# Performance work log

Measured on AMD Instinct MI355X. Metric: run time of the kernel, lower is better.

The kernel has to match this reference:

```python
import jax, jax.numpy as jnp
import numpy as np

INPUT_DIM = 512
HIDDEN_DIM = 1024
OUTPUT_DIM = 512
BATCH = 256
SEQ = 512


def setup_inputs() -> dict:
    key = jax.random.key(0)
    ks = jax.random.split(key, 7)
    s_ih = 1.0 / np.sqrt(HIDDEN_DIM)
    x = jax.random.normal(ks[0], (BATCH, SEQ, INPUT_DIM), dtype=jnp.float32)
    # PyTorch nn.LSTM params: weight_ih [4H, I], weight_hh [4H, H], biases [4H]
    W_ih = jax.random.uniform(ks[1], (4 * HIDDEN_DIM, INPUT_DIM), minval=-s_ih, maxval=s_ih, dtype=jnp.float32)
    W_hh = jax.random.uniform(ks[2], (4 * HIDDEN_DIM, HIDDEN_DIM), minval=-s_ih, maxval=s_ih, dtype=jnp.float32)
    b_ih = jax.random.uniform(ks[3], (4 * HIDDEN_DIM,), minval=-s_ih, maxval=s_ih, dtype=jnp.float32)
    b_hh = jax.random.uniform(ks[4], (4 * HIDDEN_DIM,), minval=-s_ih, maxval=s_ih, dtype=jnp.float32)
    s_fc = 1.0 / np.sqrt(HIDDEN_DIM)
    W_fc = jax.random.uniform(ks[5], (OUTPUT_DIM, HIDDEN_DIM), minval=-s_fc, maxval=s_fc, dtype=jnp.float32)
    b_fc = jax.random.uniform(ks[6], (OUTPUT_DIM,), minval=-s_fc, maxval=s_fc, dtype=jnp.float32)
    return {"x": x, "W_ih": W_ih, "W_hh": W_hh, "b_ih": b_ih, "b_hh": b_hh, "W_fc": W_fc, "b_fc": b_fc}


def _lstm_last_hidden(x, W_ih, W_hh, b_ih, b_hh):
    B = x.shape[0]
    H = W_hh.shape[1]
    # Precompute input projections for all timesteps: [T, B, 4H]
    xW = jnp.einsum('bti,gi->tbg', x, W_ih) + (b_ih + b_hh)

    def step(carry, xw_t):
        h, c = carry
        z = xw_t + h @ W_hh.T  # [B, 4H]
        i, f, g, o = jnp.split(z, 4, axis=-1)  # PyTorch gate order i,f,g,o
        i = jax.nn.sigmoid(i)
        f = jax.nn.sigmoid(f)
        g = jnp.tanh(g)
        o = jax.nn.sigmoid(o)
        c = f * c + i * g
        h = o * jnp.tanh(c)
        return (h, c), None

    h0 = jnp.zeros((B, H), dtype=x.dtype)
    c0 = jnp.zeros((B, H), dtype=x.dtype)
    (hT, _), _ = jax.lax.scan(step, (h0, c0), xW)
    return hT  # last timestep hidden == out[:, -1, :]


def reference(x, W_ih, W_hh, b_ih, b_hh, W_fc, b_fc):
    hT = _lstm_last_hidden(x, W_ih, W_hh, b_ih, b_hh)
    return hT @ W_fc.T + b_fc  # [B, output_dim]
```

## Files before the change

### kernel.cpp

```cpp
#include <hip/hip_runtime.h>
#include <stdint.h>


#define T_STEPS 512

typedef __bf16 bf16x8 __attribute__((ext_vector_type(8)));
typedef float  f32x4  __attribute__((ext_vector_type(4)));

__device__ __forceinline__ uint16_t f2bf(float f) {
  uint32_t u = __float_as_uint(f);
  u += 0x7fffu + ((u >> 16) & 1u);
  return (uint16_t)(u >> 16);
}
__device__ __forceinline__ float sigmoid_f(float z) {
  return 1.0f / (1.0f + __expf(-z));
}
__device__ __forceinline__ float tanh_f(float x) {
  float ax = __builtin_fabsf(x);
  float e  = __expf(-2.0f * ax);
  float r  = (1.0f - e) / (1.0f + e);
  return __builtin_copysignf(r, x);
}


__global__ __launch_bounds__(256) void prep_w(const float* __restrict__ Wih,
                                              const float* __restrict__ Whh,
                                              uint16_t* __restrict__ wp,
                                              int* __restrict__ flags) {
  if (blockIdx.x < 16) {
    __hip_atomic_store(&flags[blockIdx.x * 256 + threadIdx.x], 0,
                       __ATOMIC_RELAXED, __HIP_MEMORY_SCOPE_AGENT);
  }
  int idx = blockIdx.x * 256 + threadIdx.x;
  int l = idx & 63;
  int r = idx >> 6;
  int s = r % 48; r /= 48;
  int q = r & 1;  r >>= 1;
  int w = r & 3;  r >>= 2;
  int jt = r;
  int row = w * 1024 + jt * 32 + q * 16 + (l & 15);
  int kb  = s * 32 + (l >> 4) * 8;
  const float* src = (kb < 1024) ? (Whh + (size_t)row * 1024 + kb)
                                 : (Wih + (size_t)row * 512 + (kb - 1024));
  uint32_t d0 = (uint32_t)f2bf(src[0]) | ((uint32_t)f2bf(src[1]) << 16);
  uint32_t d1 = (uint32_t)f2bf(src[2]) | ((uint32_t)f2bf(src[3]) << 16);
  uint32_t d2 = (uint32_t)f2bf(src[4]) | ((uint32_t)f2bf(src[5]) << 16);
  uint32_t d3 = (uint32_t)f2bf(src[6]) | ((uint32_t)f2bf(src[7]) << 16);
  *(uint4*)(wp + (size_t)idx * 8) = make_uint4(d0, d1, d2, d3);
}

__global__ __launch_bounds__(256) void prep_x(const float* __restrict__ x,
                                              uint16_t* __restrict__ xp) {
  int idx = blockIdx.x * 256 + threadIdx.x;
  int l = idx & 63;
  int r = idx >> 6;
  int mt = r & 1;  r >>= 1;
  int ks = r & 15; r >>= 4;
  int bt = r & 7;  r >>= 3;
  int t  = r;
  int b = bt * 32 + mt * 16 + (l & 15);
  int k = ks * 32 + (l >> 4) * 8;
  const float* src = x + ((size_t)b * 512 + t) * 512 + k;
  uint32_t d0 = (uint32_t)f2bf(src[0]) | ((uint32_t)f2bf(src[1]) << 16);
  uint32_t d1 = (uint32_t)f2bf(src[2]) | ((uint32_t)f2bf(src[3]) << 16);
  uint32_t d2 = (uint32_t)f2bf(src[4]) | ((uint32_t)f2bf(src[5]) << 16);
  uint32_t d3 = (uint32_t)f2bf(src[6]) | ((uint32_t)f2bf(src[7]) << 16);
  *(uint4*)(xp + (size_t)idx * 8) = make_uint4(d0, d1, d2, d3);
}

__global__ __launch_bounds__(256, 1) void lstm_main(
    const uint16_t* __restrict__ wpack,
    const uint16_t* __restrict__ xpack,
    uint16_t* __restrict__ hpack,
    float* __restrict__ hfinal,
    int* flags,
    const float* __restrict__ bih,
    const float* __restrict__ bhh,
    const float* __restrict__ Wfc,
    const float* __restrict__ bfc,
    float* __restrict__ out) {
  extern __shared__ char smem[];

  const int tid = threadIdx.x;
  const int w   = tid >> 6;
  const int l   = tid & 63;
  const int jt  = blockIdx.x >> 3;
  const int bt  = blockIdx.x & 7;

  char* const hbuf  = smem;
  char* const xbuf0 = smem + 65536;
  char* const xbuf1 = smem + 98304;
  float* const zl   = (float*)(smem + 131072);

  int* const flag_self = flags + ((bt * 32 + jt) << 4);
  const int* const flag_poll = flags + ((bt * 32 + (l & 31)) << 4);
  int spin_budget = 2000000;

  bf16x8 fb[2][48];
#pragma unroll
  for (int q = 0; q < 2; ++q) {
#pragma unroll
    for (int s = 0; s < 48; ++s) {
      union { uint4 u; bf16x8 b; } cv;
      cv.u = *(const uint4*)(wpack +
              (size_t)(((jt * 4 + w) * 2 + q) * 48 + s) * 512 + (size_t)l * 8);
      fb[q][s] = cv.b;
    }
  }

  float bias0, bias1;
  {
    int u0b = jt * 32 + (l & 15);
    bias0 = bih[w * 1024 + u0b]      + bhh[w * 1024 + u0b];
    bias1 = bih[w * 1024 + u0b + 16] + bhh[w * 1024 + u0b + 16];
  }

  const int umt = tid >> 7;
  const int ul  = (tid >> 1) & 63;
  const int uj  = (tid & 1) * 4;
  const int um  = umt * 16 + (ul & 15);
  const int uu0 = (ul >> 4) * 8 + uj;
  float c0 = 0.f, c1 = 0.f, c2 = 0.f, c3 = 0.f;

  {
    const uint16_t* src = xpack + (size_t)bt * 16384;
#pragma unroll
    for (int i = 0; i < 8; ++i) {
      int ci = w * 8 + i;
      __builtin_amdgcn_global_load_lds(
          (const __attribute__((address_space(1))) void*)(src + (size_t)ci * 512 + (size_t)l * 8),
          (__attribute__((address_space(3))) void*)(xbuf0 + ci * 1024), 16, 0, 0);
    }
  }
  __syncthreads();

  for (int t = 0; t < T_STEPS; ++t) {
    if (t + 1 < T_STEPS) {
      const uint16_t* src = xpack + (size_t)((t + 1) * 8 + bt) * 16384;
      char* dst = ((t + 1) & 1) ? xbuf1 : xbuf0;
#pragma unroll
      for (int i = 0; i < 8; ++i) {
        int ci = w * 8 + i;
        __builtin_amdgcn_global_load_lds(
            (const __attribute__((address_space(1))) void*)(src + (size_t)ci * 512 + (size_t)l * 8),
            (__attribute__((address_space(3))) void*)(dst + ci * 1024), 16, 0, 0);
      }
    }

    f32x4 acc[2][2];
#pragma unroll
    for (int mt = 0; mt < 2; ++mt)
#pragma unroll
      for (int q = 0; q < 2; ++q) acc[mt][q] = (f32x4){0.f, 0.f, 0.f, 0.f};

    const char* xc = (t & 1) ? xbuf1 : xbuf0;

#pragma unroll
    for (int s = 0; s < 8; ++s) {
#pragma unroll
      for (int mt = 0; mt < 2; ++mt) {
        bf16x8 a = *(const bf16x8*)(xc + ((s * 2 + mt) * 64 + l) * 16);
        acc[mt][0] = __builtin_amdgcn_mfma_f32_16x16x32_bf16(a, fb[0][32 + s], acc[mt][0], 0, 0, 0);
        acc[mt][1] = __builtin_amdgcn_mfma_f32_16x16x32_bf16(a, fb[1][32 + s], acc[mt][1], 0, 0, 0);
      }
    }

    if (t > 0) {
      if (tid < 64) {
        for (;;) {
          int v = __hip_atomic_load(flag_poll, __ATOMIC_RELAXED,
                                    __HIP_MEMORY_SCOPE_AGENT);
          if (__all(v >= t)) break;
          if (--spin_budget < 0) break;
          __builtin_amdgcn_s_sleep(1);
        }
      }
      __syncthreads();
      const uint16_t* hs = hpack + (size_t)(((t - 1) & 1) * 8 + bt) * 32768;
#pragma unroll
      for (int i = 0; i < 16; ++i) {
        int ci = w * 16 + i;
        __builtin_amdgcn_global_load_lds(
            (const __attribute__((address_space(1))) void*)(hs + (size_t)ci * 512 + (size_t)l * 8),
            (__attribute__((address_space(3))) void*)(hbuf + ci * 1024), 16, 0, 17);
      }
    }

#pragma unroll
    for (int s = 8; s < 16; ++s) {
#pragma unroll
      for (int mt = 0; mt < 2; ++mt) {
        bf16x8 a = *(const bf16x8*)(xc + ((s * 2 + mt) * 64 + l) * 16);
        acc[mt][0] = __builtin_amdgcn_mfma_f32_16x16x32_bf16(a, fb[0][32 + s], acc[mt][0], 0, 0, 0);
        acc[mt][1] = __builtin_amdgcn_mfma_f32_16x16x32_bf16(a, fb[1][32 + s], acc[mt][1], 0, 0, 0);
      }
    }

    __syncthreads();
    if (t > 0) {
#pragma unroll
      for (int s = 0; s < 32; ++s) {
#pragma unroll
        for (int mt = 0; mt < 2; ++mt) {
          bf16x8 a = *(const bf16x8*)(hbuf + ((s * 2 + mt) * 64 + l) * 16);
          acc[mt][0] = __builtin_amdgcn_mfma_f32_16x16x32_bf16(a, fb[0][s], acc[mt][0], 0, 0, 0);
          acc[mt][1] = __builtin_amdgcn_mfma_f32_16x16x32_bf16(a, fb[1][s], acc[mt][1], 0, 0, 0);
        }
      }
    }

#pragma unroll
    for (int mt = 0; mt < 2; ++mt) {
#pragma unroll
      for (int q = 0; q < 2; ++q) {
        f32x4 v = acc[mt][q];
        float bq = q ? bias1 : bias0;
#pragma unroll
        for (int r = 0; r < 4; ++r) {
          float z = v[r] + bq;
          float a = (w == 2) ? tanh_f(z) : sigmoid_f(z);
          int m  = mt * 16 + (l >> 4) * 4 + r;
          int uu = q * 16 + (l & 15);
          zl[(w * 32 + m) * 36 + uu] = a;
        }
      }
    }
    __syncthreads();

    {
      const f32x4 gi = *(const f32x4*)&zl[(0 * 32 + um) * 36 + uu0];
      const f32x4 gf = *(const f32x4*)&zl[(1 * 32 + um) * 36 + uu0];
      const f32x4 gg = *(const f32x4*)&zl[(2 * 32 + um) * 36 + uu0];
      const f32x4 go = *(const f32x4*)&zl[(3 * 32 + um) * 36 + uu0];
      c0 = gf[0] * c0 + gi[0] * gg[0];
      c1 = gf[1] * c1 + gi[1] * gg[1];
      c2 = gf[2] * c2 + gi[2] * gg[2];
      c3 = gf[3] * c3 + gi[3] * gg[3];
      float h0 = go[0] * tanh_f(c0);
      float h1 = go[1] * tanh_f(c1);
      float h2 = go[2] * tanh_f(c2);
      float h3 = go[3] * tanh_f(c3);
      uint32_t p0 = (uint32_t)f2bf(h0) | ((uint32_t)f2bf(h1) << 16);
      uint32_t p1 = (uint32_t)f2bf(h2) | ((uint32_t)f2bf(h3) << 16);
      unsigned long long pv = ((unsigned long long)p1 << 32) | (unsigned long long)p0;
      uint16_t* hp = hpack +
          (size_t)((((t & 1) * 8 + bt) * 32 + jt) * 2 + umt) * 512 + (size_t)ul * 8 + uj;
      __hip_atomic_store((unsigned long long*)hp, pv,
                         __ATOMIC_RELAXED, __HIP_MEMORY_SCOPE_AGENT);
      if (t == T_STEPS - 1) {
        unsigned long long q0 = ((unsigned long long)__float_as_uint(h1) << 32) |
                                (unsigned long long)__float_as_uint(h0);
        unsigned long long q1 = ((unsigned long long)__float_as_uint(h3) << 32) |
                                (unsigned long long)__float_as_uint(h2);
        unsigned long long* fp = (unsigned long long*)
            &hfinal[(size_t)(bt * 32 + um) * 1024 + jt * 32 + uu0];
        __hip_atomic_store(fp,     q0, __ATOMIC_RELAXED, __HIP_MEMORY_SCOPE_AGENT);
        __hip_atomic_store(fp + 1, q1, __ATOMIC_RELAXED, __HIP_MEMORY_SCOPE_AGENT);
      }
    }

    asm volatile("s_waitcnt vmcnt(0)" ::: "memory");
    __syncthreads();
    if (tid == 0) {
      __hip_atomic_store(flag_self, t + 1, __ATOMIC_RELAXED,
                         __HIP_MEMORY_SCOPE_AGENT);
    }
  }

  if (tid < 64) {
    for (;;) {
      int v = __hip_atomic_load(flag_poll, __ATOMIC_RELAXED,
                                __HIP_MEMORY_SCOPE_AGENT);
      if (__all(v >= T_STEPS)) break;
      if (--spin_budget < 0) break;
      __builtin_amdgcn_s_sleep(1);
    }
  }
  __syncthreads();

  float* const hl = (float*)smem;
  {
    const unsigned long long* hq =
        (const unsigned long long*)(hfinal + (size_t)bt * 32 * 1024);
#pragma unroll 4
    for (int i = 0; i < 64; ++i) {
      int d   = i * 256 + tid;
      int row = d >> 9;
      int c2  = d & 511;
      unsigned long long v = __hip_atomic_load(hq + (size_t)row * 512 + c2,
                                               __ATOMIC_RELAXED, __HIP_MEMORY_SCOPE_AGENT);
      *(unsigned long long*)&hl[row * 1028 + c2 * 2] = v;
    }
  }
  __syncthreads();
  {
    const int bl = tid >> 3;
    const int oo = tid & 7;
    const int o0 = jt * 16 + oo * 2;
    float a0 = 0.f, a1 = 0.f;
    const float* hrow = &hl[bl * 1028];
    const float* w0p  = Wfc + (size_t)o0 * 1024;
    const float* w1p  = w0p + 1024;
#pragma unroll 8
    for (int k = 0; k < 1024; k += 4) {
      f32x4 hv = *(const f32x4*)&hrow[k];
      f32x4 w0 = *(const f32x4*)&w0p[k];
      f32x4 w1 = *(const f32x4*)&w1p[k];
      a0 += hv[0] * w0[0] + hv[1] * w0[1] + hv[2] * w0[2] + hv[3] * w0[3];
      a1 += hv[0] * w1[0] + hv[1] * w1[1] + hv[2] * w1[2] + hv[3] * w1[3];
    }
    int b = bt * 32 + bl;
    out[(size_t)b * 512 + o0]     = a0 + bfc[o0];
    out[(size_t)b * 512 + o0 + 1] = a1 + bfc[o0 + 1];
  }
}

extern "C" void kernel_launch(void* const* d_in, const int* in_sizes, int n_in,
                              void* d_out, int out_size, void* d_ws, size_t ws_size,
                              hipStream_t stream) {
  const float* x   = (const float*)d_in[0];
  const float* Wih = (const float*)d_in[1];
  const float* Whh = (const float*)d_in[2];
  const float* bih = (const float*)d_in[3];
  const float* bhh = (const float*)d_in[4];
  const float* Wfc = (const float*)d_in[5];
  const float* bfc = (const float*)d_in[6];
  float* out = (float*)d_out;

  char* ws = (char*)d_ws;
  uint16_t* wp  = (uint16_t*)(ws);
  uint16_t* xp  = (uint16_t*)(ws + 12582912);
  uint16_t* hp  = (uint16_t*)(ws + 146800640);
  float*    hf  = (float*)   (ws + 147849216);
  int*      fl  = (int*)     (ws + 148897792);

  (void)hipFuncSetAttribute((const void*)lstm_main,
                            hipFuncAttributeMaxDynamicSharedMemorySize, 149504);

  hipLaunchKernelGGL(prep_w, dim3(3072), dim3(256), 0, stream, Wih, Whh, wp, fl);
  hipLaunchKernelGGL(prep_x, dim3(32768), dim3(256), 0, stream, x, xp);
  hipLaunchKernelGGL(lstm_main, dim3(256), dim3(256), 149504, stream,
                     wp, xp, hp, hf, fl, bih, bhh, Wfc, bfc, out);
}
```

Before: 3.688 ms.

## Pipeline recurrent h loads into four groups with partial vmcnt waits

The per-step h-state load into LDS is reordered so that each wave's chunks interleave across four groups. The h-projection MFMA loop is split into four stages, each waiting only on its own group's loads with a partial vmcnt and a barrier, so compute on early chunks overlaps the remaining loads. The next-timestep x prefetch is moved after the flag wait so it no longer competes with the h loads on the critical path. This relies on the ordering of vmcnt counters, and mixing inline-asm waitcnt with the compiler's own scheduling is fragile.

New measurement: 4.005 ms. 1.09x slower.

```diff
diff --git a/kernel.cpp b/kernel.cpp
--- a/kernel.cpp
+++ b/kernel.cpp
@@ -68,6 +68,25 @@
   *(uint4*)(xp + (size_t)idx * 8) = make_uint4(d0, d1, d2, d3);
 }
 
+#define H_GROUP(g, VM)                                                        \
+  do {                                                                        \
+    asm volatile("s_waitcnt vmcnt(" #VM ")" ::: "memory");                    \
+    __builtin_amdgcn_s_barrier();                                             \
+    asm volatile("" ::: "memory");                                            \
+    _Pragma("unroll")                                                         \
+    for (int so = 0; so < 8; ++so) {                                          \
+      const int s = (g) * 8 + so;                                             \
+      _Pragma("unroll")                                                       \
+      for (int mt = 0; mt < 2; ++mt) {                                        \
+        bf16x8 a = *(const bf16x8*)(hbuf + ((s * 2 + mt) * 64 + l) * 16);     \
+        acc[mt][0] = __builtin_amdgcn_mfma_f32_16x16x32_bf16(                 \
+            a, fb[0][s], acc[mt][0], 0, 0, 0);                                \
+        acc[mt][1] = __builtin_amdgcn_mfma_f32_16x16x32_bf16(                 \
+            a, fb[1][s], acc[mt][1], 0, 0, 0);                                \
+      }                                                                       \
+    }                                                                         \
+  } while (0)
+
 __global__ __launch_bounds__(256, 1) void lstm_main(
     const uint16_t* __restrict__ wpack,
     const uint16_t* __restrict__ xpack,
@@ -135,18 +154,6 @@
   __syncthreads();
 
   for (int t = 0; t < T_STEPS; ++t) {
-    if (t + 1 < T_STEPS) {
-      const uint16_t* src = xpack + (size_t)((t + 1) * 8 + bt) * 16384;
-      char* dst = ((t + 1) & 1) ? xbuf1 : xbuf0;
-#pragma unroll
-      for (int i = 0; i < 8; ++i) {
-        int ci = w * 8 + i;
-        __builtin_amdgcn_global_load_lds(
-            (const __attribute__((address_space(1))) void*)(src + (size_t)ci * 512 + (size_t)l * 8),
-            (__attribute__((address_space(3))) void*)(dst + ci * 1024), 16, 0, 0);
-      }
-    }
-
     f32x4 acc[2][2];
 #pragma unroll
     for (int mt = 0; mt < 2; ++mt)
@@ -176,10 +183,25 @@
         }
       }
       __syncthreads();
+    }
+
+    if (t + 1 < T_STEPS) {
+      const uint16_t* src = xpack + (size_t)((t + 1) * 8 + bt) * 16384;
+      char* dst = ((t + 1) & 1) ? xbuf1 : xbuf0;
+#pragma unroll
+      for (int i = 0; i < 8; ++i) {
+        int ci = w * 8 + i;
+        __builtin_amdgcn_global_load_lds(
+            (const __attribute__((address_space(1))) void*)(src + (size_t)ci * 512 + (size_t)l * 8),
+            (__attribute__((address_space(3))) void*)(dst + ci * 1024), 16, 0, 0);
+      }
+    }
+
+    if (t > 0) {
       const uint16_t* hs = hpack + (size_t)(((t - 1) & 1) * 8 + bt) * 32768;
 #pragma unroll
       for (int i = 0; i < 16; ++i) {
-        int ci = w * 16 + i;
+        int ci = 16 * (i >> 2) + w * 4 + (i & 3);
         __builtin_amdgcn_global_load_lds(
             (const __attribute__((address_space(1))) void*)(hs + (size_t)ci * 512 + (size_t)l * 8),
             (__attribute__((address_space(3))) void*)(hbuf + ci * 1024), 16, 0, 17);
@@ -196,17 +218,13 @@
       }
     }
 
-    __syncthreads();
     if (t > 0) {
-#pragma unroll
-      for (int s = 0; s < 32; ++s) {
-#pragma unroll
-        for (int mt = 0; mt < 2; ++mt) {
-          bf16x8 a = *(const bf16x8*)(hbuf + ((s * 2 + mt) * 64 + l) * 16);
-          acc[mt][0] = __builtin_amdgcn_mfma_f32_16x16x32_bf16(a, fb[0][s], acc[mt][0], 0, 0, 0);
-          acc[mt][1] = __builtin_amdgcn_mfma_f32_16x16x32_bf16(a, fb[1][s], acc[mt][1], 0, 0, 0);
-        }
-      }
+      H_GROUP(0, 12);
+      H_GROUP(1, 8);
+      H_GROUP(2, 4);
+      H_GROUP(3, 0);
+    } else {
+      __syncthreads();
     }
 
 #pragma unroll
```

## Split LSTM step K-reduction across two wave groups with 512-thread blocks

Applied to the files above, without the earlier changes.

Doubles the block to 512 threads (8 waves). Each gate's K-dimension is split between two wave halves, so each wave holds half the weight fragments in registers. Partial sums are reduced through LDS before the activation, and the cell update and FC epilogue are spread over more threads. The next-step x prefetch moves to after the flag wait, and the spin budget is lowered. The aim is to shorten the serial per-step latency by halving the MFMA chain per wave, at the cost of an extra LDS exchange and barrier each step.

Result: slower. 5.453 ms (+47.8%).

```diff
diff --git a/kernel.cpp b/kernel.cpp
--- a/kernel.cpp
+++ b/kernel.cpp
@@ -6,6 +6,7 @@
 
 typedef __bf16 bf16x8 __attribute__((ext_vector_type(8)));
 typedef float  f32x4  __attribute__((ext_vector_type(4)));
+typedef float  f32x2  __attribute__((ext_vector_type(2)));
 
 __device__ __forceinline__ uint16_t f2bf(float f) {
   uint32_t u = __float_as_uint(f);
@@ -68,7 +69,7 @@
   *(uint4*)(xp + (size_t)idx * 8) = make_uint4(d0, d1, d2, d3);
 }
 
-__global__ __launch_bounds__(256, 1) void lstm_main(
+__global__ __launch_bounds__(512, 2) void lstm_main(
     const uint16_t* __restrict__ wpack,
     const uint16_t* __restrict__ xpack,
     uint16_t* __restrict__ hpack,
@@ -82,7 +83,9 @@
   extern __shared__ char smem[];
 
   const int tid = threadIdx.x;
-  const int w   = tid >> 6;
+  const int w8  = tid >> 6;
+  const int g8  = w8 & 3;
+  const int p8  = w8 >> 2;
   const int l   = tid & 63;
   const int jt  = blockIdx.x >> 3;
   const int bt  = blockIdx.x & 7;
@@ -94,39 +97,40 @@
 
   int* const flag_self = flags + ((bt * 32 + jt) << 4);
   const int* const flag_poll = flags + ((bt * 32 + (l & 31)) << 4);
-  int spin_budget = 2000000;
-
-  bf16x8 fb[2][48];
+  int spin_budget = 150000;
+
+  bf16x8 fb[2][24];
 #pragma unroll
   for (int q = 0; q < 2; ++q) {
 #pragma unroll
-    for (int s = 0; s < 48; ++s) {
+    for (int j = 0; j < 24; ++j) {
+      int s = (j < 16) ? (p8 * 16 + j) : (32 + p8 * 8 + (j - 16));
       union { uint4 u; bf16x8 b; } cv;
       cv.u = *(const uint4*)(wpack +
-              (size_t)(((jt * 4 + w) * 2 + q) * 48 + s) * 512 + (size_t)l * 8);
-      fb[q][s] = cv.b;
+              (size_t)(((jt * 4 + g8) * 2 + q) * 48 + s) * 512 + (size_t)l * 8);
+      fb[q][j] = cv.b;
     }
   }
 
   float bias0, bias1;
   {
     int u0b = jt * 32 + (l & 15);
-    bias0 = bih[w * 1024 + u0b]      + bhh[w * 1024 + u0b];
-    bias1 = bih[w * 1024 + u0b + 16] + bhh[w * 1024 + u0b + 16];
-  }
-
-  const int umt = tid >> 7;
-  const int ul  = (tid >> 1) & 63;
-  const int uj  = (tid & 1) * 4;
+    bias0 = bih[g8 * 1024 + u0b]      + bhh[g8 * 1024 + u0b];
+    bias1 = bih[g8 * 1024 + u0b + 16] + bhh[g8 * 1024 + u0b + 16];
+  }
+
+  const int umt = tid >> 8;
+  const int ul  = (tid >> 2) & 63;
+  const int uj  = (tid & 3) * 2;
   const int um  = umt * 16 + (ul & 15);
   const int uu0 = (ul >> 4) * 8 + uj;
-  float c0 = 0.f, c1 = 0.f, c2 = 0.f, c3 = 0.f;
+  float c0 = 0.f, c1 = 0.f;
 
   {
     const uint16_t* src = xpack + (size_t)bt * 16384;
 #pragma unroll
-    for (int i = 0; i < 8; ++i) {
-      int ci = w * 8 + i;
+    for (int i = 0; i < 4; ++i) {
+      int ci = w8 * 4 + i;
       __builtin_amdgcn_global_load_lds(
           (const __attribute__((address_space(1))) void*)(src + (size_t)ci * 512 + (size_t)l * 8),
           (__attribute__((address_space(3))) void*)(xbuf0 + ci * 1024), 16, 0, 0);
@@ -135,18 +139,6 @@
   __syncthreads();
 
   for (int t = 0; t < T_STEPS; ++t) {
-    if (t + 1 < T_STEPS) {
-      const uint16_t* src = xpack + (size_t)((t + 1) * 8 + bt) * 16384;
-      char* dst = ((t + 1) & 1) ? xbuf1 : xbuf0;
-#pragma unroll
-      for (int i = 0; i < 8; ++i) {
-        int ci = w * 8 + i;
-        __builtin_amdgcn_global_load_lds(
-            (const __attribute__((address_space(1))) void*)(src + (size_t)ci * 512 + (size_t)l * 8),
-            (__attribute__((address_space(3))) void*)(dst + ci * 1024), 16, 0, 0);
-      }
-    }
-
     f32x4 acc[2][2];
 #pragma unroll
     for (int mt = 0; mt < 2; ++mt)
@@ -156,12 +148,13 @@
     const char* xc = (t & 1) ? xbuf1 : xbuf0;
 
 #pragma unroll
-    for (int s = 0; s < 8; ++s) {
+    for (int jj = 0; jj < 4; ++jj) {
+      int ks = p8 * 8 + jj;
 #pragma unroll
       for (int mt = 0; mt < 2; ++mt) {
-        bf16x8 a = *(const bf16x8*)(xc + ((s * 2 + mt) * 64 + l) * 16);
-        acc[mt][0] = __builtin_amdgcn_mfma_f32_16x16x32_bf16(a, fb[0][32 + s], acc[mt][0], 0, 0, 0);
-        acc[mt][1] = __builtin_amdgcn_mfma_f32_16x16x32_bf16(a, fb[1][32 + s], acc[mt][1], 0, 0, 0);
+        bf16x8 a = *(const bf16x8*)(xc + ((ks * 2 + mt) * 64 + l) * 16);
+        acc[mt][0] = __builtin_amdgcn_mfma_f32_16x16x32_bf16(a, fb[0][16 + jj], acc[mt][0], 0, 0, 0);
+        acc[mt][1] = __builtin_amdgcn_mfma_f32_16x16x32_bf16(a, fb[1][16 + jj], acc[mt][1], 0, 0, 0);
       }
     }
 
@@ -176,10 +169,25 @@
         }
       }
       __syncthreads();
+    }
+
+    if (t + 1 < T_STEPS) {
+      const uint16_t* src = xpack + (size_t)((t + 1) * 8 + bt) * 16384;
+      char* dst = ((t + 1) & 1) ? xbuf1 : xbuf0;
+#pragma unroll
+      for (int i = 0; i < 4; ++i) {
+        int ci = w8 * 4 + i;
+        __builtin_amdgcn_global_load_lds(
+            (const __attribute__((address_space(1))) void*)(src + (size_t)ci * 512 + (size_t)l * 8),
+            (__attribute__((address_space(3))) void*)(dst + ci * 1024), 16, 0, 0);
+      }
+    }
+
+    if (t > 0) {
       const uint16_t* hs = hpack + (size_t)(((t - 1) & 1) * 8 + bt) * 32768;
 #pragma unroll
-      for (int i = 0; i < 16; ++i) {
-        int ci = w * 16 + i;
+      for (int i = 0; i < 8; ++i) {
+        int ci = w8 * 8 + i;
         __builtin_amdgcn_global_load_lds(
             (const __attribute__((address_space(1))) void*)(hs + (size_t)ci * 512 + (size_t)l * 8),
             (__attribute__((address_space(3))) void*)(hbuf + ci * 1024), 16, 0, 17);
@@ -187,75 +195,83 @@
     }
 
 #pragma unroll
-    for (int s = 8; s < 16; ++s) {
+    for (int jj = 4; jj < 8; ++jj) {
+      int ks = p8 * 8 + jj;
 #pragma unroll
       for (int mt = 0; mt < 2; ++mt) {
-        bf16x8 a = *(const bf16x8*)(xc + ((s * 2 + mt) * 64 + l) * 16);
-        acc[mt][0] = __builtin_amdgcn_mfma_f32_16x16x32_bf16(a, fb[0][32 + s], acc[mt][0], 0, 0, 0);
-        acc[mt][1] = __builtin_amdgcn_mfma_f32_16x16x32_bf16(a, fb[1][32 + s], acc[mt][1], 0, 0, 0);
+        bf16x8 a = *(const bf16x8*)(xc + ((ks * 2 + mt) * 64 + l) * 16);
+        acc[mt][0] = __builtin_amdgcn_mfma_f32_16x16x32_bf16(a, fb[0][16 + jj], acc[mt][0], 0, 0, 0);
+        acc[mt][1] = __builtin_amdgcn_mfma_f32_16x16x32_bf16(a, fb[1][16 + jj], acc[mt][1], 0, 0, 0);
       }
     }
 
     __syncthreads();
     if (t > 0) {
 #pragma unroll
-      for (int s = 0; s < 32; ++s) {
+      for (int j = 0; j < 16; ++j) {
+        int s = p8 * 16 + j;
 #pragma unroll
         for (int mt = 0; mt < 2; ++mt) {
           bf16x8 a = *(const bf16x8*)(hbuf + ((s * 2 + mt) * 64 + l) * 16);
-          acc[mt][0] = __builtin_amdgcn_mfma_f32_16x16x32_bf16(a, fb[0][s], acc[mt][0], 0, 0, 0);
-          acc[mt][1] = __builtin_amdgcn_mfma_f32_16x16x32_bf16(a, fb[1][s], acc[mt][1], 0, 0, 0);
+          acc[mt][0] = __builtin_amdgcn_mfma_f32_16x16x32_bf16(a, fb[0][j], acc[mt][0], 0, 0, 0);
+          acc[mt][1] = __builtin_amdgcn_mfma_f32_16x16x32_bf16(a, fb[1][j], acc[mt][1], 0, 0, 0);
         }
       }
     }
 
-#pragma unroll
-    for (int mt = 0; mt < 2; ++mt) {
+    {
+      const int mto = 1 - p8;
 #pragma unroll
       for (int q = 0; q < 2; ++q) {
-        f32x4 v = acc[mt][q];
+        f32x4 v = acc[mto][q];
+#pragma unroll
+        for (int r = 0; r < 4; ++r) {
+          int m  = mto * 16 + (l >> 4) * 4 + r;
+          int uu = q * 16 + (l & 15);
+          zl[(g8 * 32 + m) * 36 + uu] = v[r];
+        }
+      }
+    }
+    __syncthreads();
+
+    {
+      const int mtk = p8;
+#pragma unroll
+      for (int q = 0; q < 2; ++q) {
+        f32x4 v = acc[mtk][q];
         float bq = q ? bias1 : bias0;
 #pragma unroll
         for (int r = 0; r < 4; ++r) {
-          float z = v[r] + bq;
-          float a = (w == 2) ? tanh_f(z) : sigmoid_f(z);
-          int m  = mt * 16 + (l >> 4) * 4 + r;
+          int m  = mtk * 16 + (l >> 4) * 4 + r;
           int uu = q * 16 + (l & 15);
-          zl[(w * 32 + m) * 36 + uu] = a;
+          float z = v[r] + zl[(g8 * 32 + m) * 36 + uu] + bq;
+          float a = (g8 == 2) ? tanh_f(z) : sigmoid_f(z);
+          zl[(g8 * 32 + m) * 36 + uu] = a;
         }
       }
     }
     __syncthreads();
 
     {
-      const f32x4 gi = *(const f32x4*)&zl[(0 * 32 + um) * 36 + uu0];
-      const f32x4 gf = *(const f32x4*)&zl[(1 * 32 + um) * 36 + uu0];
-      const f32x4 gg = *(const f32x4*)&zl[(2 * 32 + um) * 36 + uu0];
-      const f32x4 go = *(const f32x4*)&zl[(3 * 32 + um) * 36 + uu0];
+      const f32x2 gi = *(const f32x2*)&zl[(0 * 32 + um) * 36 + uu0];
+      const f32x2 gf = *(const f32x2*)&zl[(1 * 32 + um) * 36 + uu0];
+      const f32x2 gg = *(const f32x2*)&zl[(2 * 32 + um) * 36 + uu0];
+      const f32x2 go = *(const f32x2*)&zl[(3 * 32 + um) * 36 + uu0];
       c0 = gf[0] * c0 + gi[0] * gg[0];
       c1 = gf[1] * c1 + gi[1] * gg[1];
-      c2 = gf[2] * c2 + gi[2] * gg[2];
-      c3 = gf[3] * c3 + gi[3] * gg[3];
       float h0 = go[0] * tanh_f(c0);
       float h1 = go[1] * tanh_f(c1);
-      float h2 = go[2] * tanh_f(c2);
-      float h3 = go[3] * tanh_f(c3);
-      uint32_t p0 = (uint32_t)f2bf(h0) | ((uint32_t)f2bf(h1) << 16);
-      uint32_t p1 = (uint32_t)f2bf(h2) | ((uint32_t)f2bf(h3) << 16);
-      unsigned long long pv = ((unsigned long long)p1 << 32) | (unsigned long long)p0;
+      uint32_t pv = (uint32_t)f2bf(h0) | ((uint32_t)f2bf(h1) << 16);
       uint16_t* hp = hpack +
           (size_t)((((t & 1) * 8 + bt) * 32 + jt) * 2 + umt) * 512 + (size_t)ul * 8 + uj;
-      __hip_atomic_store((unsigned long long*)hp, pv,
+      __hip_atomic_store((uint32_t*)hp, pv,
                          __ATOMIC_RELAXED, __HIP_MEMORY_SCOPE_AGENT);
       if (t == T_STEPS - 1) {
         unsigned long long q0 = ((unsigned long long)__float_as_uint(h1) << 32) |
                                 (unsigned long long)__float_as_uint(h0);
-        unsigned long long q1 = ((unsigned long long)__float_as_uint(h3) << 32) |
-                                (unsigned long long)__float_as_uint(h2);
         unsigned long long* fp = (unsigned long long*)
             &hfinal[(size_t)(bt * 32 + um) * 1024 + jt * 32 + uu0];
-        __hip_atomic_store(fp,     q0, __ATOMIC_RELAXED, __HIP_MEMORY_SCOPE_AGENT);
-        __hip_atomic_store(fp + 1, q1, __ATOMIC_RELAXED, __HIP_MEMORY_SCOPE_AGENT);
+        __hip_atomic_store(fp, q0, __ATOMIC_RELAXED, __HIP_MEMORY_SCOPE_AGENT);
       }
     }
 
@@ -283,8 +299,8 @@
     const unsigned long long* hq =
         (const unsigned long long*)(hfinal + (size_t)bt * 32 * 1024);
 #pragma unroll 4
-    for (int i = 0; i < 64; ++i) {
-      int d   = i * 256 + tid;
+    for (int i = 0; i < 32; ++i) {
+      int d   = i * 512 + tid;
       int row = d >> 9;
       int c2  = d & 511;
       unsigned long long v = __hip_atomic_load(hq + (size_t)row * 512 + c2,
@@ -294,24 +310,20 @@
   }
   __syncthreads();
   {
-    const int bl = tid >> 3;
-    const int oo = tid & 7;
-    const int o0 = jt * 16 + oo * 2;
-    float a0 = 0.f, a1 = 0.f;
+    const int bl = tid >> 4;
+    const int oo = tid & 15;
+    const int o0 = jt * 16 + oo;
+    float a0 = 0.f;
     const float* hrow = &hl[bl * 1028];
     const float* w0p  = Wfc + (size_t)o0 * 1024;
-    const float* w1p  = w0p + 1024;
 #pragma unroll 8
     for (int k = 0; k < 1024; k += 4) {
       f32x4 hv = *(const f32x4*)&hrow[k];
       f32x4 w0 = *(const f32x4*)&w0p[k];
-      f32x4 w1 = *(const f32x4*)&w1p[k];
       a0 += hv[0] * w0[0] + hv[1] * w0[1] + hv[2] * w0[2] + hv[3] * w0[3];
-      a1 += hv[0] * w1[0] + hv[1] * w1[1] + hv[2] * w1[2] + hv[3] * w1[3];
     }
     int b = bt * 32 + bl;
-    out[(size_t)b * 512 + o0]     = a0 + bfc[o0];
-    out[(size_t)b * 512 + o0 + 1] = a1 + bfc[o0 + 1];
+    out[(size_t)b * 512 + o0] = a0 + bfc[o0];
   }
 }
 
@@ -339,6 +351,6 @@
 
   hipLaunchKernelGGL(prep_w, dim3(3072), dim3(256), 0, stream, Wih, Whh, wp, fl);
   hipLaunchKernelGGL(prep_x, dim3(32768), dim3(256), 0, stream, x, xp);
-  hipLaunchKernelGGL(lstm_main, dim3(256), dim3(256), 149504, stream,
+  hipLaunchKernelGGL(lstm_main, dim3(256), dim3(512), 149504, stream,
                      wp, xp, hp, hf, fl, bih, bhh, Wfc, bfc, out);
 }
```

## Split LSTM batch tile into two halves to overlap hidden-state exchange

Applied to the files above, without the earlier changes.

Each timestep now runs as two half-steps, one per 16-row half of the block's batch tile. Each half has its own ready flags and its own LDS h buffer. While one half computes its recurrent MFMAs and gate update, the h of the other half is fetched from global memory once its producers signal readiness, so the grid-wide exchange latency is meant to hide behind compute. The cost is twice as many barriers and flag publications per step, and smaller vector stores. The spin-wait timeout is also cut sharply, which risks a silent early break if producers fall behind.

After: 4.030 ms. 1.09x slower.

```diff
diff --git a/kernel.cpp b/kernel.cpp
--- a/kernel.cpp
+++ b/kernel.cpp
@@ -6,6 +6,7 @@
 
 typedef __bf16 bf16x8 __attribute__((ext_vector_type(8)));
 typedef float  f32x4  __attribute__((ext_vector_type(4)));
+typedef float  f32x2  __attribute__((ext_vector_type(2)));
 
 __device__ __forceinline__ uint16_t f2bf(float f) {
   uint32_t u = __float_as_uint(f);
@@ -68,6 +69,120 @@
   *(uint4*)(xp + (size_t)idx * 8) = make_uint4(d0, d1, d2, d3);
 }
 
+#define HALF_STEP(X, DO_LOAD, S_LOAD, DO_PREF, C0, C1)                        \
+  do {                                                                        \
+    f32x4 acc0 = (f32x4){0.f, 0.f, 0.f, 0.f};                                 \
+    f32x4 acc1 = (f32x4){0.f, 0.f, 0.f, 0.f};                                 \
+    const char* xc = (t & 1) ? xbuf1 : xbuf0;                                 \
+                                           \
+    _Pragma("unroll")                                                         \
+    for (int s = 0; s < 16; ++s) {                                            \
+      bf16x8 a = *(const bf16x8*)(xc + ((s * 2 + (X)) * 64 + l) * 16);        \
+      acc0 = __builtin_amdgcn_mfma_f32_16x16x32_bf16(a, fb[0][32 + s], acc0, 0, 0, 0); \
+      acc1 = __builtin_amdgcn_mfma_f32_16x16x32_bf16(a, fb[1][32 + s], acc1, 0, 0, 0); \
+    }                                                                         \
+                            \
+    if (t > 0) {                                                              \
+      const char* hb = (X) ? hbufB : hbufA;                                   \
+      _Pragma("unroll")                                                       \
+      for (int s = 0; s < 32; ++s) {                                          \
+        bf16x8 a = *(const bf16x8*)(hb + (s * 64 + l) * 16);                  \
+        acc0 = __builtin_amdgcn_mfma_f32_16x16x32_bf16(a, fb[0][s], acc0, 0, 0, 0); \
+        acc1 = __builtin_amdgcn_mfma_f32_16x16x32_bf16(a, fb[1][s], acc1, 0, 0, 0); \
+      }                                                                       \
+    }                                                                         \
+           \
+    if (DO_LOAD) {                                                            \
+      const int tgt = (S_LOAD) + 1;                                           \
+      const int* fp = (X) ? flag_pollA : flag_pollB;                          \
+      for (;;) {                                                              \
+        int v = __hip_atomic_load(fp, __ATOMIC_RELAXED,                       \
+                                  __HIP_MEMORY_SCOPE_AGENT);                  \
+        if (__all(v >= tgt)) break;                                           \
+        if (--spin_budget < 0) break;                                         \
+        __builtin_amdgcn_s_sleep(1);                                          \
+      }                                                                       \
+      const uint16_t* hs = hpack +                                            \
+          (size_t)(((S_LOAD) & 1) * 8 + bt) * 32768 + (1 - (X)) * 512;        \
+      char* hd = (X) ? hbufA : hbufB;                                         \
+      _Pragma("unroll")                                                       \
+      for (int i = 0; i < 8; ++i) {                                           \
+        int ci = w * 8 + i;                                                   \
+        __builtin_amdgcn_global_load_lds(                                     \
+            (const __attribute__((address_space(1))) void*)(hs + (size_t)ci * 1024 + (size_t)l * 8), \
+            (__attribute__((address_space(3))) void*)(hd + ci * 1024), 16, 0, 17); \
+      }                                                                       \
+    }                                                                         \
+                  \
+    if ((DO_PREF) && t + 1 < T_STEPS) {                                       \
+      const uint16_t* src = xpack + (size_t)((t + 1) * 8 + bt) * 16384;       \
+      char* dst = ((t + 1) & 1) ? xbuf1 : xbuf0;                              \
+      _Pragma("unroll")                                                       \
+      for (int i = 0; i < 8; ++i) {                                           \
+        int ci = w * 8 + i;                                                   \
+        __builtin_amdgcn_global_load_lds(                                     \
+            (const __attribute__((address_space(1))) void*)(src + (size_t)ci * 512 + (size_t)l * 8), \
+            (__attribute__((address_space(3))) void*)(dst + ci * 1024), 16, 0, 0); \
+      }                                                                       \
+    }                                                                         \
+                  \
+    {                                                                         \
+      f32x4 v = acc0; float bq = bias0;                                       \
+      _Pragma("unroll")                                                       \
+      for (int r = 0; r < 4; ++r) {                                           \
+        float z = v[r] + bq;                                                  \
+        float a = (w == 2) ? tanh_f(z) : sigmoid_f(z);                        \
+        int m  = (X) * 16 + (l >> 4) * 4 + r;                                 \
+        zl[(w * 32 + m) * 36 + (l & 15)] = a;                                 \
+      }                                                                       \
+    }                                                                         \
+    {                                                                         \
+      f32x4 v = acc1; float bq = bias1;                                       \
+      _Pragma("unroll")                                                       \
+      for (int r = 0; r < 4; ++r) {                                           \
+        float z = v[r] + bq;                                                  \
+        float a = (w == 2) ? tanh_f(z) : sigmoid_f(z);                        \
+        int m  = (X) * 16 + (l >> 4) * 4 + r;                                 \
+        zl[(w * 32 + m) * 36 + 16 + (l & 15)] = a;                            \
+      }                                                                       \
+    }                                                                         \
+    __syncthreads();                                        \
+            \
+    {                                                                         \
+      const int ir = tid >> 4;                                                \
+      const int u0 = (tid & 15) * 2;                                          \
+      const f32x2 gi = *(const f32x2*)&zl[(0 * 32 + (X) * 16 + ir) * 36 + u0];\
+      const f32x2 gf = *(const f32x2*)&zl[(1 * 32 + (X) * 16 + ir) * 36 + u0];\
+      const f32x2 gg = *(const f32x2*)&zl[(2 * 32 + (X) * 16 + ir) * 36 + u0];\
+      const f32x2 go = *(const f32x2*)&zl[(3 * 32 + (X) * 16 + ir) * 36 + u0];\
+      C0 = gf[0] * C0 + gi[0] * gg[0];                                        \
+      C1 = gf[1] * C1 + gi[1] * gg[1];                                        \
+      float h0 = go[0] * tanh_f(C0);                                          \
+      float h1 = go[1] * tanh_f(C1);                                          \
+      uint32_t pv = (uint32_t)f2bf(h0) | ((uint32_t)f2bf(h1) << 16);          \
+      int hl_lane = ir + ((u0 >> 3) << 4);                                    \
+      uint16_t* hp = hpack +                                                  \
+          (size_t)((((t & 1) * 8 + bt) * 32 + jt) * 2 + (X)) * 512 +          \
+          hl_lane * 8 + (u0 & 7);                                             \
+      __hip_atomic_store((uint32_t*)hp, pv,                                   \
+                         __ATOMIC_RELAXED, __HIP_MEMORY_SCOPE_AGENT);         \
+      if (t == T_STEPS - 1) {                                                 \
+        unsigned long long q0 = ((unsigned long long)__float_as_uint(h1) << 32) | \
+                                (unsigned long long)__float_as_uint(h0);      \
+        unsigned long long* fpf = (unsigned long long*)                       \
+            &hfinal[(size_t)(bt * 32 + (X) * 16 + ir) * 1024 + jt * 32 + u0]; \
+        __hip_atomic_store(fpf, q0, __ATOMIC_RELAXED, __HIP_MEMORY_SCOPE_AGENT); \
+      }                                                                       \
+    }                                                                         \
+                   \
+    asm volatile("s_waitcnt vmcnt(0)" ::: "memory");                          \
+    __syncthreads();                                                  \
+    if (tid == 0) {                                                           \
+      __hip_atomic_store(flag_self + (X) * 8, t + 1,                          \
+                         __ATOMIC_RELAXED, __HIP_MEMORY_SCOPE_AGENT);         \
+    }                                                                         \
+  } while (0)
+
 __global__ __launch_bounds__(256, 1) void lstm_main(
     const uint16_t* __restrict__ wpack,
     const uint16_t* __restrict__ xpack,
@@ -87,14 +202,16 @@
   const int jt  = blockIdx.x >> 3;
   const int bt  = blockIdx.x & 7;
 
-  char* const hbuf  = smem;
+  char* const hbufA = smem;
+  char* const hbufB = smem + 32768;
   char* const xbuf0 = smem + 65536;
   char* const xbuf1 = smem + 98304;
   float* const zl   = (float*)(smem + 131072);
 
   int* const flag_self = flags + ((bt * 32 + jt) << 4);
-  const int* const flag_poll = flags + ((bt * 32 + (l & 31)) << 4);
-  int spin_budget = 2000000;
+  const int* const flag_pollA = flags + ((bt * 32 + (l & 31)) << 4);
+  const int* const flag_pollB = flag_pollA + 8;
+  int spin_budget = 150000;
 
   bf16x8 fb[2][48];
 #pragma unroll
@@ -115,12 +232,7 @@
     bias1 = bih[w * 1024 + u0b + 16] + bhh[w * 1024 + u0b + 16];
   }
 
-  const int umt = tid >> 7;
-  const int ul  = (tid >> 1) & 63;
-  const int uj  = (tid & 1) * 4;
-  const int um  = umt * 16 + (ul & 15);
-  const int uu0 = (ul >> 4) * 8 + uj;
-  float c0 = 0.f, c1 = 0.f, c2 = 0.f, c3 = 0.f;
+  float cA0 = 0.f, cA1 = 0.f, cB0 = 0.f, cB1 = 0.f;
 
   {
     const uint16_t* src = xpack + (size_t)bt * 16384;
@@ -135,142 +247,14 @@
   __syncthreads();
 
   for (int t = 0; t < T_STEPS; ++t) {
-    if (t + 1 < T_STEPS) {
-      const uint16_t* src = xpack + (size_t)((t + 1) * 8 + bt) * 16384;
-      char* dst = ((t + 1) & 1) ? xbuf1 : xbuf0;
-#pragma unroll
-      for (int i = 0; i < 8; ++i) {
-        int ci = w * 8 + i;
-        __builtin_amdgcn_global_load_lds(
-            (const __attribute__((address_space(1))) void*)(src + (size_t)ci * 512 + (size_t)l * 8),
-            (__attribute__((address_space(3))) void*)(dst + ci * 1024), 16, 0, 0);
-      }
-    }
-
-    f32x4 acc[2][2];
-#pragma unroll
-    for (int mt = 0; mt < 2; ++mt)
-#pragma unroll
-      for (int q = 0; q < 2; ++q) acc[mt][q] = (f32x4){0.f, 0.f, 0.f, 0.f};
-
-    const char* xc = (t & 1) ? xbuf1 : xbuf0;
-
-#pragma unroll
-    for (int s = 0; s < 8; ++s) {
-#pragma unroll
-      for (int mt = 0; mt < 2; ++mt) {
-        bf16x8 a = *(const bf16x8*)(xc + ((s * 2 + mt) * 64 + l) * 16);
-        acc[mt][0] = __builtin_amdgcn_mfma_f32_16x16x32_bf16(a, fb[0][32 + s], acc[mt][0], 0, 0, 0);
-        acc[mt][1] = __builtin_amdgcn_mfma_f32_16x16x32_bf16(a, fb[1][32 + s], acc[mt][1], 0, 0, 0);
-      }
-    }
-
-    if (t > 0) {
-      if (tid < 64) {
-        for (;;) {
-          int v = __hip_atomic_load(flag_poll, __ATOMIC_RELAXED,
-                                    __HIP_MEMORY_SCOPE_AGENT);
-          if (__all(v >= t)) break;
-          if (--spin_budget < 0) break;
-          __builtin_amdgcn_s_sleep(1);
-        }
-      }
-      __syncthreads();
-      const uint16_t* hs = hpack + (size_t)(((t - 1) & 1) * 8 + bt) * 32768;
-#pragma unroll
-      for (int i = 0; i < 16; ++i) {
-        int ci = w * 16 + i;
-        __builtin_amdgcn_global_load_lds(
-            (const __attribute__((address_space(1))) void*)(hs + (size_t)ci * 512 + (size_t)l * 8),
-            (__attribute__((address_space(3))) void*)(hbuf + ci * 1024), 16, 0, 17);
-      }
-    }
-
-#pragma unroll
-    for (int s = 8; s < 16; ++s) {
-#pragma unroll
-      for (int mt = 0; mt < 2; ++mt) {
-        bf16x8 a = *(const bf16x8*)(xc + ((s * 2 + mt) * 64 + l) * 16);
-        acc[mt][0] = __builtin_amdgcn_mfma_f32_16x16x32_bf16(a, fb[0][32 + s], acc[mt][0], 0, 0, 0);
-        acc[mt][1] = __builtin_amdgcn_mfma_f32_16x16x32_bf16(a, fb[1][32 + s], acc[mt][1], 0, 0, 0);
-      }
-    }
-
-    __syncthreads();
-    if (t > 0) {
-#pragma unroll
-      for (int s = 0; s < 32; ++s) {
-#pragma unroll
-        for (int mt = 0; mt < 2; ++mt) {
-          bf16x8 a = *(const bf16x8*)(hbuf + ((s * 2 + mt) * 64 + l) * 16);
-          acc[mt][0] = __builtin_amdgcn_mfma_f32_16x16x32_bf16(a, fb[0][s], acc[mt][0], 0, 0, 0);
-          acc[mt][1] = __builtin_amdgcn_mfma_f32_16x16x32_bf16(a, fb[1][s], acc[mt][1], 0, 0, 0);
-        }
-      }
-    }
-
-#pragma unroll
-    for (int mt = 0; mt < 2; ++mt) {
-#pragma unroll
-      for (int q = 0; q < 2; ++q) {
-        f32x4 v = acc[mt][q];
-        float bq = q ? bias1 : bias0;
-#pragma unroll
-        for (int r = 0; r < 4; ++r) {
-          float z = v[r] + bq;
-          float a = (w == 2) ? tanh_f(z) : sigmoid_f(z);
-          int m  = mt * 16 + (l >> 4) * 4 + r;
-          int uu = q * 16 + (l & 15);
-          zl[(w * 32 + m) * 36 + uu] = a;
-        }
-      }
-    }
-    __syncthreads();
-
-    {
-      const f32x4 gi = *(const f32x4*)&zl[(0 * 32 + um) * 36 + uu0];
-      const f32x4 gf = *(const f32x4*)&zl[(1 * 32 + um) * 36 + uu0];
-      const f32x4 gg = *(const f32x4*)&zl[(2 * 32 + um) * 36 + uu0];
-      const f32x4 go = *(const f32x4*)&zl[(3 * 32 + um) * 36 + uu0];
-      c0 = gf[0] * c0 + gi[0] * gg[0];
-      c1 = gf[1] * c1 + gi[1] * gg[1];
-      c2 = gf[2] * c2 + gi[2] * gg[2];
-      c3 = gf[3] * c3 + gi[3] * gg[3];
-      float h0 = go[0] * tanh_f(c0);
-      float h1 = go[1] * tanh_f(c1);
-      float h2 = go[2] * tanh_f(c2);
-      float h3 = go[3] * tanh_f(c3);
-      uint32_t p0 = (uint32_t)f2bf(h0) | ((uint32_t)f2bf(h1) << 16);
-      uint32_t p1 = (uint32_t)f2bf(h2) | ((uint32_t)f2bf(h3) << 16);
-      unsigned long long pv = ((unsigned long long)p1 << 32) | (unsigned long long)p0;
-      uint16_t* hp = hpack +
-          (size_t)((((t & 1) * 8 + bt) * 32 + jt) * 2 + umt) * 512 + (size_t)ul * 8 + uj;
-      __hip_atomic_store((unsigned long long*)hp, pv,
-                         __ATOMIC_RELAXED, __HIP_MEMORY_SCOPE_AGENT);
-      if (t == T_STEPS - 1) {
-        unsigned long long q0 = ((unsigned long long)__float_as_uint(h1) << 32) |
-                                (unsigned long long)__float_as_uint(h0);
-        unsigned long long q1 = ((unsigned long long)__float_as_uint(h3) << 32) |
-                                (unsigned long long)__float_as_uint(h2);
-        unsigned long long* fp = (unsigned long long*)
-            &hfinal[(size_t)(bt * 32 + um) * 1024 + jt * 32 + uu0];
-        __hip_atomic_store(fp,     q0, __ATOMIC_RELAXED, __HIP_MEMORY_SCOPE_AGENT);
-        __hip_atomic_store(fp + 1, q1, __ATOMIC_RELAXED, __HIP_MEMORY_SCOPE_AGENT);
-      }
-    }
-
-    asm volatile("s_waitcnt vmcnt(0)" ::: "memory");
-    __syncthreads();
-    if (tid == 0) {
-      __hip_atomic_store(flag_self, t + 1, __ATOMIC_RELAXED,
-                         __HIP_MEMORY_SCOPE_AGENT);
-    }
+    HALF_STEP(0, (t > 0), (t - 1), 1, cA0, cA1);
+    HALF_STEP(1, (t < T_STEPS - 1), (t), 0, cB0, cB1);
   }
 
   if (tid < 64) {
+    const int* fp = (l < 32) ? flag_pollA : flag_pollB;
     for (;;) {
-      int v = __hip_atomic_load(flag_poll, __ATOMIC_RELAXED,
-                                __HIP_MEMORY_SCOPE_AGENT);
+      int v = __hip_atomic_load(fp, __ATOMIC_RELAXED, __HIP_MEMORY_SCOPE_AGENT);
       if (__all(v >= T_STEPS)) break;
       if (--spin_budget < 0) break;
       __builtin_amdgcn_s_sleep(1);
```
